# Optimization experiments

Measured on AMD Instinct MI355X. Metric: run time of the kernel, lower is better.

Reference implementation:

```python
import jax, jax.numpy as jnp
import numpy as np

N_NODES = 100000
N_EDGES = 3200000
IN_F = 256
OUT_F = 128
NEG_SLOPE = 0.2


def setup_inputs() -> dict:
    key = jax.random.key(0)
    k1, k2, k3, k4, k5 = jax.random.split(key, 5)
    features = jax.random.normal(k1, (N_NODES, IN_F), dtype=jnp.float32)
    # xavier-uniform-ish linear weight [out, in]
    limit = float(np.sqrt(6.0 / (IN_F + OUT_F)))
    weight = jax.random.uniform(k2, (OUT_F, IN_F), dtype=jnp.float32, minval=-limit, maxval=limit)
    edge_vals = jax.random.uniform(k3, (N_EDGES,), dtype=jnp.float32)
    edge_rows = jax.random.randint(k4, (N_EDGES,), 0, N_NODES, dtype=jnp.int32)
    edge_cols = jax.random.randint(k5, (N_EDGES,), 0, N_NODES, dtype=jnp.int32)
    return {"features": features, "weight": weight, "edge_vals": edge_vals,
            "edge_rows": edge_rows, "edge_cols": edge_cols}


def reference(features, weight, edge_vals, edge_rows, edge_cols):
    # support = LeakyReLU(features @ W^T)   (active=True path)
    support = jax.nn.leaky_relu(jnp.einsum('ni,oi->no', features, weight), NEG_SLOPE)
    # output = spmm(adj, support): out[r] += v_e * support[c_e]
    gathered = support[edge_cols] * edge_vals[:, None]   # [E, out]
    out = jax.ops.segment_sum(gathered, edge_rows, num_segments=N_NODES)
    return out
```

## Files before the change

### kernel.cpp

```cpp
#include <hip/hip_runtime.h>
#include <hip/hip_bf16.h>

#define N_NODES 100000
#define N_EDGES 3200000
#define IN_F 256
#define OUT_F 128
#define NEG_SLOPE 0.2f
#define NB 782
#define CHUNK 4096
#define NPB 782
#define BCAP 4608

typedef short s16x8 __attribute__((ext_vector_type(8)));
typedef float f32x4 __attribute__((ext_vector_type(4)));
typedef float f32x2v __attribute__((ext_vector_type(2)));
typedef unsigned u32x2 __attribute__((ext_vector_type(2)));

__device__ __forceinline__ unsigned short f2bf(float f) {
    __bf16 h = (__bf16)f;
    return __builtin_bit_cast(unsigned short, h);
}
__device__ __forceinline__ float bf2f(unsigned short u) {
    unsigned int x = ((unsigned int)u) << 16;
    return __builtin_bit_cast(float, x);
}

__global__ void wcvt_kernel(const float* __restrict__ w, unsigned short* __restrict__ wb) {
    int t = blockIdx.x * blockDim.x + threadIdx.x;
    if (t >= (OUT_F / 16) * (IN_F / 32) * 64) return;
    int lane = t & 63;
    int nt   = (t >> 6) & 7;
    int kit  = t >> 9;
    int l16  = lane & 15;
    int quad = lane >> 4;
    const float* src = w + (nt * 16 + l16) * IN_F + kit * 32 + quad * 8;
    float4 v0 = *(const float4*)src;
    float4 v1 = *(const float4*)(src + 4);
    ushort4 o0, o1;
    o0.x = f2bf(v0.x); o0.y = f2bf(v0.y); o0.z = f2bf(v0.z); o0.w = f2bf(v0.w);
    o1.x = f2bf(v1.x); o1.y = f2bf(v1.y); o1.z = f2bf(v1.z); o1.w = f2bf(v1.w);
    *(ushort4*)(wb + t * 8)     = o0;
    *(ushort4*)(wb + t * 8 + 4) = o1;
}

__global__ __launch_bounds__(256) void gemm_kernel(
    const float* __restrict__ feat, const unsigned short* __restrict__ wb,
    unsigned short* __restrict__ sup) {
    int wid  = threadIdx.x >> 6;
    int lane = threadIdx.x & 63;
    long m0 = ((long)blockIdx.x * 4 + wid) * 16;
    if (m0 >= N_NODES) return;
    int quad = lane >> 4;
    int l16  = lane & 15;
    int kq   = quad * 8;

    const float* arow = feat + (m0 + l16) * IN_F + kq;

    f32x4 acc[8];
#pragma unroll
    for (int nt = 0; nt < 8; ++nt) acc[nt] = (f32x4){0.f, 0.f, 0.f, 0.f};

#pragma unroll
    for (int k0 = 0; k0 < IN_F; k0 += 32) {
        f32x4 a0 = __builtin_nontemporal_load((const f32x4*)(arow + k0));
        f32x4 a1 = __builtin_nontemporal_load((const f32x4*)(arow + k0 + 4));
        s16x8 a;
        a[0] = (short)f2bf(a0[0]); a[1] = (short)f2bf(a0[1]);
        a[2] = (short)f2bf(a0[2]); a[3] = (short)f2bf(a0[3]);
        a[4] = (short)f2bf(a1[0]); a[5] = (short)f2bf(a1[1]);
        a[6] = (short)f2bf(a1[2]); a[7] = (short)f2bf(a1[3]);
        const unsigned short* wp = wb + (k0 >> 5) * 4096 + lane * 8;
#pragma unroll
        for (int nt = 0; nt < 8; ++nt) {
            s16x8 b = *(const s16x8*)(wp + nt * 512);
            acc[nt] = __builtin_amdgcn_mfma_f32_16x16x32_bf16(a, b, acc[nt], 0, 0, 0);
        }
    }

    int crow = (int)m0 + quad * 4;
#pragma unroll
    for (int nt = 0; nt < 8; ++nt) {
#pragma unroll
        for (int r = 0; r < 4; ++r) {
            float v = acc[nt][r];
            v = (v > 0.f) ? v : (NEG_SLOPE * v);
            sup[(long)(crow + r) * OUT_F + nt * 16 + l16] = f2bf(v);
        }
    }
}

__global__ __launch_bounds__(256) void hist_kernel(const int* __restrict__ rows,
                                                   int* __restrict__ gcnt) {
    __shared__ int lh[NB];
    int t = threadIdx.x;
    for (int s = t; s < NB; s += 256) lh[s] = 0;
    __syncthreads();
    int e0 = blockIdx.x * CHUNK;
    int m = N_EDGES - e0; if (m > CHUNK) m = CHUNK;
    for (int k = t; k < m; k += 256)
        atomicAdd(&lh[__builtin_nontemporal_load(rows + e0 + k) >> 7], 1);
    __syncthreads();
    for (int s = t; s < NB; s += 256)
        gcnt[s * NPB + blockIdx.x] = lh[s];
}

__global__ __launch_bounds__(256) void scan_kernel(int* __restrict__ gcnt,
                                                   int* __restrict__ bcnt) {
    __shared__ int st[256];
    int s = blockIdx.x, t = threadIdx.x;
    int* row = gcnt + (long)s * NPB;
    int v[4]; int sum = 0;
#pragma unroll
    for (int k = 0; k < 4; ++k) {
        int i = t * 4 + k;
        v[k] = (i < NPB) ? row[i] : 0;
        sum += v[k];
    }
    st[t] = sum;
    __syncthreads();
    for (int o = 1; o < 256; o <<= 1) {
        int x = (t >= o) ? st[t - o] : 0;
        __syncthreads();
        st[t] += x;
        __syncthreads();
    }
    int run = st[t] - sum;
#pragma unroll
    for (int k = 0; k < 4; ++k) {
        int i = t * 4 + k;
        if (i < NPB) row[i] = run;
        run += v[k];
    }
    if (t == 255) bcnt[s] = run;
}

__global__ __launch_bounds__(256) void mscatter_kernel(const int* __restrict__ rows,
    const int* __restrict__ cols, const float* __restrict__ vals,
    const int* __restrict__ boff, uint2* __restrict__ ed) {
    __shared__ int lhist[NB];
    __shared__ int lbase[NB];
    int t = threadIdx.x;
    for (int s = t; s < NB; s += 256) lhist[s] = 0;
    __syncthreads();
    int e0 = blockIdx.x * CHUNK;
    int m = N_EDGES - e0; if (m > CHUNK) m = CHUNK;

    int rk[16]; int rr[16]; unsigned cw[16], vw[16];
#pragma unroll
    for (int k = 0; k < 16; ++k) {
        int i = k * 256 + t;
        if (i < m) {
            int e = e0 + i;
            int r = __builtin_nontemporal_load(rows + e);
            rr[k] = r;
            cw[k] = (unsigned)__builtin_nontemporal_load(cols + e);
            vw[k] = __builtin_bit_cast(unsigned, __builtin_nontemporal_load(vals + e));
            rk[k] = atomicAdd(&lhist[r >> 7], 1);
        }
    }
    __syncthreads();
    for (int s = t; s < NB; s += 256)
        lbase[s] = boff[(long)s * NPB + blockIdx.x];
    __syncthreads();
#pragma unroll
    for (int k = 0; k < 16; ++k) {
        int i = k * 256 + t;
        if (i < m) {
            int r  = rr[k];
            int b  = r >> 7;
            int g  = lbase[b] + rk[k];
            if (g < BCAP) {
                uint2 e;
                e.x = ((unsigned)(r & 127) << 17) | cw[k];
                e.y = vw[k];
                ed[(long)b * BCAP + g] = e;
            }
        }
    }
}

__global__ __launch_bounds__(512) void gather_kernel(const uint2* __restrict__ ed,
    const int* __restrict__ bcnt,
    const unsigned short* __restrict__ sup, float* __restrict__ out, int b0) {
    __shared__ uint2 stage[BCAP];
    __shared__ int h[128];
    __shared__ int bs[128];
    __shared__ int cur[128];
    int t = threadIdx.x;
    int bkt = b0 + blockIdx.x;
    if (t < 128) h[t] = 0;
    __syncthreads();
    int n = bcnt[bkt]; if (n > BCAP) n = BCAP;
    const uint2* p = ed + (long)bkt * BCAP;

    uint2 er[9];
#pragma unroll
    for (int k = 0; k < 9; ++k) {
        int i = k * 512 + t;
        if (i < n) {
            u32x2 v = __builtin_nontemporal_load((const u32x2*)(p + i));
            er[k].x = v[0]; er[k].y = v[1];
        }
    }
#pragma unroll
    for (int k = 0; k < 9; ++k) {
        int i = k * 512 + t;
        if (i < n) atomicAdd(&h[er[k].x >> 17], 1);
    }
    __syncthreads();

    if (t < 128) bs[t] = h[t];
    __syncthreads();
    for (int o = 1; o < 128; o <<= 1) {
        int v = 0;
        if (t < 128 && t >= o) v = bs[t - o];
        __syncthreads();
        if (t < 128) bs[t] += v;
        __syncthreads();
    }
    if (t < 128) {
        int excl = bs[t] - h[t];
        bs[t] = excl;
        cur[t] = excl;
    }
    __syncthreads();

#pragma unroll
    for (int k = 0; k < 9; ++k) {
        int i = k * 512 + t;
        if (i < n) {
            int rl = er[k].x >> 17;
            int pos = atomicAdd(&cur[rl], 1);
            stage[pos] = er[k];
        }
    }
    __syncthreads();

    int wid = t >> 6, lane = t & 63;
    long rowbase = (long)bkt * 128;

#define PROC(E) {                                                            \
        int col = (E).x & 0x1FFFF;                                           \
        float v = __builtin_bit_cast(float, (E).y);                          \
        ushort2 s2 = *(const ushort2*)(sup + (long)col * OUT_F + lane * 2);  \
        a0 += v * bf2f(s2.x); a1 += v * bf2f(s2.y);                          \
    }

    for (int rq = 0; rq < 16; ++rq) {
        int lr = wid * 16 + rq;
        int s0 = bs[lr];
        int mm = h[lr];
        float a0 = 0.f, a1 = 0.f;
        int i = 0;
        for (; i + 16 <= mm; i += 16) {
            uint2 e[16];
#pragma unroll
            for (int k = 0; k < 16; ++k) e[k] = stage[s0 + i + k];
#pragma unroll
            for (int k = 0; k < 16; ++k) PROC(e[k]);
        }
        for (; i + 8 <= mm; i += 8) {
            uint2 e0 = stage[s0 + i],     e1 = stage[s0 + i + 1];
            uint2 e2 = stage[s0 + i + 2], e3 = stage[s0 + i + 3];
            uint2 e4 = stage[s0 + i + 4], e5 = stage[s0 + i + 5];
            uint2 e6 = stage[s0 + i + 6], e7 = stage[s0 + i + 7];
            PROC(e0); PROC(e1); PROC(e2); PROC(e3);
            PROC(e4); PROC(e5); PROC(e6); PROC(e7);
        }
        for (; i < mm; ++i) { uint2 e0 = stage[s0 + i]; PROC(e0); }
        long grow = rowbase + lr;
        if (grow < N_NODES) {
            f32x2v f; f[0] = a0; f[1] = a1;
            __builtin_nontemporal_store(f, (f32x2v*)(out + grow * OUT_F + lane * 2));
        }
    }
#undef PROC
}

extern "C" void kernel_launch(void* const* d_in, const int* in_sizes, int n_in,
                              void* d_out, int out_size, void* d_ws, size_t ws_size,
                              hipStream_t stream) {
    const float* feat  = (const float*)d_in[0];
    const float* w     = (const float*)d_in[1];
    const float* evals = (const float*)d_in[2];
    const int*   erows = (const int*)d_in[3];
    const int*   ecols = (const int*)d_in[4];
    float* out = (float*)d_out;

    char* p = (char*)d_ws;
    unsigned short* wb  = (unsigned short*)p;  p += 65536;
    unsigned short* sup = (unsigned short*)p;  p += (size_t)N_NODES * OUT_F * 2;
    int* gcnt   = (int*)p;                     p += (size_t)NB * NPB * 4;
    int* bcnt   = (int*)p;                     p += 4096;
    uint2* ed   = (uint2*)p;

    wcvt_kernel<<<16, 256, 0, stream>>>(w, wb);

    int gemm_blocks = (N_NODES / 16 + 3) / 4;
    gemm_kernel<<<gemm_blocks, 256, 0, stream>>>(feat, wb, sup);

    hist_kernel<<<NPB, 256, 0, stream>>>(erows, gcnt);
    scan_kernel<<<NB, 256, 0, stream>>>(gcnt, bcnt);
    mscatter_kernel<<<NPB, 256, 0, stream>>>(erows, ecols, evals, gcnt, ed);

    int q = NB / 4;
    gather_kernel<<<q, 512, 0, stream>>>(ed, bcnt, sup, out, 0);
    gather_kernel<<<q, 512, 0, stream>>>(ed, bcnt, sup, out, q);
    gather_kernel<<<q, 512, 0, stream>>>(ed, bcnt, sup, out, 2 * q);
    gather_kernel<<<NB - 3 * q, 512, 0, stream>>>(ed, bcnt, sup, out, 3 * q);
}
```

Baseline: 468.7 us.

## Split each gather bucket across two blocks and simplify scatter/hist kernels

The gather stage now launches two blocks per 128-row bucket, each handling 64 rows with a smaller shared staging buffer, and replaces the four sequential launches with a single launch. This raises block count and occupancy, but each block still loads and filters the whole bucket's edge list, so the edge reads are doubled. Its row scan becomes a wavefront shuffle scan in place of the barrier-based one. The scatter kernel becomes a single pass that loads bases up front, dropping the register staging and one barrier. The histogram kernel uses int4 loads.

Result: faster. 395.0 us (-15.7%).

```diff
diff --git a/kernel.cpp b/kernel.cpp
--- a/kernel.cpp
+++ b/kernel.cpp
@@ -10,6 +10,7 @@
 #define CHUNK 4096
 #define NPB 782
 #define BCAP 4608
+#define SCAP 2560
 
 typedef short s16x8 __attribute__((ext_vector_type(8)));
 typedef float f32x4 __attribute__((ext_vector_type(4)));
@@ -97,11 +98,16 @@
     __syncthreads();
     int e0 = blockIdx.x * CHUNK;
     int m = N_EDGES - e0; if (m > CHUNK) m = CHUNK;
-    for (int k = t; k < m; k += 256)
-        atomicAdd(&lh[__builtin_nontemporal_load(rows + e0 + k) >> 7], 1);
+    for (int k = t * 4; k < m; k += 1024) {
+        int4 r4 = *(const int4*)(rows + e0 + k);
+        atomicAdd(&lh[r4.x >> 7], 1);
+        atomicAdd(&lh[r4.y >> 7], 1);
+        atomicAdd(&lh[r4.z >> 7], 1);
+        atomicAdd(&lh[r4.w >> 7], 1);
+    }
     __syncthreads();
     for (int s = t; s < NB; s += 256)
-        gcnt[s * NPB + blockIdx.x] = lh[s];
+        gcnt[(long)s * NPB + blockIdx.x] = lh[s];
 }
 
 __global__ __launch_bounds__(256) void scan_kernel(int* __restrict__ gcnt,
@@ -140,55 +146,42 @@
     __shared__ int lhist[NB];
     __shared__ int lbase[NB];
     int t = threadIdx.x;
-    for (int s = t; s < NB; s += 256) lhist[s] = 0;
+    for (int s = t; s < NB; s += 256) {
+        lhist[s] = 0;
+        lbase[s] = boff[(long)s * NPB + blockIdx.x];
+    }
     __syncthreads();
     int e0 = blockIdx.x * CHUNK;
     int m = N_EDGES - e0; if (m > CHUNK) m = CHUNK;
-
-    int rk[16]; int rr[16]; unsigned cw[16], vw[16];
-#pragma unroll
-    for (int k = 0; k < 16; ++k) {
-        int i = k * 256 + t;
-        if (i < m) {
-            int e = e0 + i;
-            int r = __builtin_nontemporal_load(rows + e);
-            rr[k] = r;
-            cw[k] = (unsigned)__builtin_nontemporal_load(cols + e);
-            vw[k] = __builtin_bit_cast(unsigned, __builtin_nontemporal_load(vals + e));
-            rk[k] = atomicAdd(&lhist[r >> 7], 1);
-        }
-    }
-    __syncthreads();
-    for (int s = t; s < NB; s += 256)
-        lbase[s] = boff[(long)s * NPB + blockIdx.x];
-    __syncthreads();
-#pragma unroll
-    for (int k = 0; k < 16; ++k) {
-        int i = k * 256 + t;
-        if (i < m) {
-            int r  = rr[k];
-            int b  = r >> 7;
-            int g  = lbase[b] + rk[k];
-            if (g < BCAP) {
-                uint2 e;
-                e.x = ((unsigned)(r & 127) << 17) | cw[k];
-                e.y = vw[k];
-                ed[(long)b * BCAP + g] = e;
-            }
+#pragma unroll 4
+    for (int i = t; i < m; i += 256) {
+        int e = e0 + i;
+        int r      = __builtin_nontemporal_load(rows + e);
+        unsigned c = (unsigned)__builtin_nontemporal_load(cols + e);
+        unsigned v = __builtin_bit_cast(unsigned, __builtin_nontemporal_load(vals + e));
+        int b  = r >> 7;
+        int rk = atomicAdd(&lhist[b], 1);
+        int g  = lbase[b] + rk;
+        if (g < BCAP) {
+            uint2 ee;
+            ee.x = ((unsigned)(r & 127) << 17) | c;
+            ee.y = v;
+            ed[(long)b * BCAP + g] = ee;
         }
     }
 }
 
 __global__ __launch_bounds__(512) void gather_kernel(const uint2* __restrict__ ed,
     const int* __restrict__ bcnt,
-    const unsigned short* __restrict__ sup, float* __restrict__ out, int b0) {
-    __shared__ uint2 stage[BCAP];
-    __shared__ int h[128];
-    __shared__ int bs[128];
-    __shared__ int cur[128];
+    const unsigned short* __restrict__ sup, float* __restrict__ out) {
+    __shared__ uint2 stage[SCAP];
+    __shared__ int h[64];
+    __shared__ int bs[64];
+    __shared__ int cur[64];
     int t = threadIdx.x;
-    int bkt = b0 + blockIdx.x;
-    if (t < 128) h[t] = 0;
+    int bkt  = blockIdx.x >> 1;
+    int half = blockIdx.x & 1;
+    if (t < 64) h[t] = 0;
     __syncthreads();
     int n = bcnt[bkt]; if (n > BCAP) n = BCAP;
     const uint2* p = ed + (long)bkt * BCAP;
@@ -205,23 +198,23 @@
 #pragma unroll
     for (int k = 0; k < 9; ++k) {
         int i = k * 512 + t;
-        if (i < n) atomicAdd(&h[er[k].x >> 17], 1);
-    }
-    __syncthreads();
-
-    if (t < 128) bs[t] = h[t];
-    __syncthreads();
-    for (int o = 1; o < 128; o <<= 1) {
-        int v = 0;
-        if (t < 128 && t >= o) v = bs[t - o];
-        __syncthreads();
-        if (t < 128) bs[t] += v;
-        __syncthreads();
-    }
-    if (t < 128) {
-        int excl = bs[t] - h[t];
-        bs[t] = excl;
-        cur[t] = excl;
+        if (i < n) {
+            int rl = er[k].x >> 17;
+            if ((rl >> 6) == half) atomicAdd(&h[rl & 63], 1);
+        }
+    }
+    __syncthreads();
+
+    if (t < 64) {
+        int v = h[t];
+        int orig = v;
+#pragma unroll
+        for (int o = 1; o < 64; o <<= 1) {
+            int u = __shfl_up(v, o, 64);
+            if (t >= o) v += u;
+        }
+        bs[t] = v - orig;
+        cur[t] = v - orig;
     }
     __syncthreads();
 
@@ -230,14 +223,16 @@
         int i = k * 512 + t;
         if (i < n) {
             int rl = er[k].x >> 17;
-            int pos = atomicAdd(&cur[rl], 1);
-            stage[pos] = er[k];
+            if ((rl >> 6) == half) {
+                int pos = atomicAdd(&cur[rl & 63], 1);
+                if (pos < SCAP) stage[pos] = er[k];
+            }
         }
     }
     __syncthreads();
 
     int wid = t >> 6, lane = t & 63;
-    long rowbase = (long)bkt * 128;
+    long rowbase = (long)bkt * 128 + half * 64;
 
 #define PROC(E) {                                                            \
         int col = (E).x & 0x1FFFF;                                           \
@@ -246,10 +241,11 @@
         a0 += v * bf2f(s2.x); a1 += v * bf2f(s2.y);                          \
     }
 
-    for (int rq = 0; rq < 16; ++rq) {
-        int lr = wid * 16 + rq;
+    for (int rq = 0; rq < 8; ++rq) {
+        int lr = wid * 8 + rq;
         int s0 = bs[lr];
         int mm = h[lr];
+        if (s0 + mm > SCAP) mm = SCAP - s0;
         float a0 = 0.f, a1 = 0.f;
         int i = 0;
         for (; i + 16 <= mm; i += 16) {
@@ -303,9 +299,5 @@
     scan_kernel<<<NB, 256, 0, stream>>>(gcnt, bcnt);
     mscatter_kernel<<<NPB, 256, 0, stream>>>(erows, ecols, evals, gcnt, ed);
 
-    int q = NB / 4;
-    gather_kernel<<<q, 512, 0, stream>>>(ed, bcnt, sup, out, 0);
-    gather_kernel<<<q, 512, 0, stream>>>(ed, bcnt, sup, out, q);
-    gather_kernel<<<q, 512, 0, stream>>>(ed, bcnt, sup, out, 2 * q);
-    gather_kernel<<<NB - 3 * q, 512, 0, stream>>>(ed, bcnt, sup, out, 3 * q);
-}
+    gather_kernel<<<NB * 2, 512, 0, stream>>>(ed, bcnt, sup, out);
+}
```
